# Performance work log

Measured on AMD Instinct MI355X. Metric: run time of the kernel, lower is better.

## Reference

```python
import jax, jax.numpy as jnp
import numpy as np

B, S, N, H, C = 64, 512, 24, 768, 6

CONST_LAST = jnp.array([0.1, 0.1, 0.1, 0.3, 0.8, 0.01], dtype=jnp.float32)
CONST_MID = jnp.array([0.1, 0.1, 0.1, 0.8, 0.3, 0.01], dtype=jnp.float32)


def setup_inputs() -> dict:
    key = jax.random.key(0)
    k1, k2, k3, k4 = jax.random.split(key, 4)
    last_hidden_state = jax.random.normal(k1, (B, S, H), dtype=jnp.float32)
    # strictly increasing boundaries in [0, S-1]: sort randint in [0, S-N) then add arange(N)
    base = jnp.sort(jax.random.randint(k2, (B, N), 0, S - N), axis=1)
    sentence_token = base + jnp.arange(N, dtype=base.dtype)[None, :]
    W = jax.random.normal(k3, (C, H), dtype=jnp.float32) * 0.02
    b = jax.random.normal(k4, (C,), dtype=jnp.float32) * 0.02
    return {"last_hidden_state": last_hidden_state, "sentence_token": sentence_token,
            "W": W, "b": b}


def reference(last_hidden_state, sentence_token, W, b):
    # last_hidden_state: [B,S,H]; sentence_token: [B,N] strictly increasing boundaries.
    # Segment j covers tokens [prev+1, t_j] inclusive (prev = -1 for j==0).
    ends = sentence_token                                            # [B,N]
    prev = jnp.concatenate([-jnp.ones_like(ends[:, :1]), ends[:, :-1]], axis=1)
    # prefix sums with leading zero: csp[:, t+1] = sum of tokens 0..t
    cs = jnp.cumsum(last_hidden_state, axis=1)                       # [B,S,H]
    csp = jnp.concatenate([jnp.zeros_like(cs[:, :1]), cs], axis=1)   # [B,S+1,H]
    seg_sum = (jnp.take_along_axis(csp, (ends + 1)[:, :, None], axis=1)
               - jnp.take_along_axis(csp, (prev + 1)[:, :, None], axis=1))  # [B,N,H]
    lens = (ends - prev).astype(last_hidden_state.dtype)[:, :, None]  # >= 1 by construction
    seg_mean = seg_sum / lens                                         # [B,N,H]
    probs = jax.nn.sigmoid(jnp.einsum('bnh,ch->bnc', seg_mean, W) + b)  # [B,N,C]
    # override: boundary > 500 -> constant probability vector (different if last sentence)
    is_last = (jnp.arange(ends.shape[1]) == ends.shape[1] - 1)[None, :, None]  # [1,N,1]
    const = jnp.where(is_last, CONST_LAST[None, None, :], CONST_MID[None, None, :])
    over = (ends > 500)[:, :, None]
    return jnp.where(over, const, probs)
```

## Files before the change

### kernel.cpp

```cpp
#include <hip/hip_runtime.h>
#include <math.h>

#define B_ 64
#define S_ 512
#define N_ 24
#define H_ 768
#define C_ 6
#define CHUNKS 16
#define TOK_PER_BLOCK (S_ / CHUNKS)
#define TOK_PER_WAVE (TOK_PER_BLOCK / 4)

__global__ __launch_bounds__(256, 4) void seg_proj_kernel(
    const float* __restrict__ lhs, const int* __restrict__ st,
    const float* __restrict__ W, float* __restrict__ outbuf, int use_atomic) {
  __shared__ float acc[N_ * C_ * 64];
  const int tid = threadIdx.x;
  const int lane = tid & 63;
  const int wave = tid >> 6;
  const int b = blockIdx.x / CHUNKS;
  const int chunk = blockIdx.x % CHUNKS;

  float4* accv = (float4*)acc;
#pragma unroll
  for (int i = 0; i < 9; ++i)
    accv[i * 256 + tid] = make_float4(0.f, 0.f, 0.f, 0.f);

  int stb_l = (lane < N_) ? st[b * N_ + lane] : 0x7fffffff;
  const int last = __shfl(stb_l, N_ - 1);
  const int lim = last > 500 ? 500 : last;

  const float4* W4 = (const float4*)W;
  float4 w[3][C_];
#pragma unroll
  for (int k = 0; k < 3; ++k)
#pragma unroll
    for (int c = 0; c < C_; ++c)
      w[k][c] = W4[c * (H_ / 4) + k * 64 + lane];
#pragma unroll
  for (int k = 0; k < 3; ++k)
    asm volatile("" : "+v"(w[k][0].x), "+v"(w[k][0].y), "+v"(w[k][0].z), "+v"(w[k][0].w),
                       "+v"(w[k][1].x), "+v"(w[k][1].y), "+v"(w[k][1].z), "+v"(w[k][1].w),
                       "+v"(w[k][2].x), "+v"(w[k][2].y), "+v"(w[k][2].z), "+v"(w[k][2].w),
                       "+v"(w[k][3].x), "+v"(w[k][3].y), "+v"(w[k][3].z), "+v"(w[k][3].w),
                       "+v"(w[k][4].x), "+v"(w[k][4].y), "+v"(w[k][4].z), "+v"(w[k][4].w),
                       "+v"(w[k][5].x), "+v"(w[k][5].y), "+v"(w[k][5].z), "+v"(w[k][5].w));

  __syncthreads();

  const int s_base = chunk * TOK_PER_BLOCK + wave * TOK_PER_WAVE;
  if (s_base <= lim) {
    const float4* x4 = (const float4*)(lhs + ((size_t)b * S_ + s_base) * H_);
    float4 x[TOK_PER_WAVE][3];
#pragma unroll
    for (int t = 0; t < TOK_PER_WAVE; ++t) {
      x[t][0] = x4[t * 192 + lane];
      x[t][1] = x4[t * 192 + 64 + lane];
      x[t][2] = x4[t * 192 + 128 + lane];
    }

    float racc[C_] = {0.f, 0.f, 0.f, 0.f, 0.f, 0.f};
    int cur_seg = N_;
#pragma unroll
    for (int t = 0; t < TOK_PER_WAVE; ++t) {
      const int s = s_base + t;
      const int seg = (int)__popcll(__ballot(stb_l < s));
      if (seg != cur_seg) {
        if (cur_seg < N_) {
#pragma unroll
        for (int c = 0; c < C_; ++c)
          atomicAdd(&acc[(cur_seg * C_ + c) * 64 + lane], racc[c]);
        }
#pragma unroll
        for (int c = 0; c < C_; ++c) racc[c] = 0.f;
        cur_seg = seg;
      }
#pragma unroll
      for (int k = 0; k < 3; ++k)
#pragma unroll
        for (int c = 0; c < C_; ++c)
          racc[c] += x[t][k].x * w[k][c].x + x[t][k].y * w[k][c].y +
                     x[t][k].z * w[k][c].z + x[t][k].w * w[k][c].w;
    }
    if (cur_seg < N_) {
#pragma unroll
      for (int c = 0; c < C_; ++c)
        atomicAdd(&acc[(cur_seg * C_ + c) * 64 + lane], racc[c]);
    }
  }

  __syncthreads();
  if (tid < N_ * C_) {
    float v = 0.f;
    const int base = tid * 64;
#pragma unroll 8
    for (int i = 0; i < 64; ++i) v += acc[base + ((i + tid) & 63)];
    if (use_atomic)
      atomicAdd(&outbuf[b * N_ * C_ + tid], v);
    else
      outbuf[(size_t)blockIdx.x * (N_ * C_) + tid] = v;
  }
}

__global__ __launch_bounds__(256) void finalize_kernel(
    const float* __restrict__ buf, const int* __restrict__ st,
    const float* __restrict__ bias, float* __restrict__ out, int use_atomic) {
  int idx = blockIdx.x * blockDim.x + threadIdx.x;
  if (idx >= B_ * N_ * C_) return;
  int c = idx % C_;
  int j = (idx / C_) % N_;
  int b = idx / (N_ * C_);
  float ssum;
  if (use_atomic) {
    ssum = buf[idx];
  } else {
    ssum = 0.f;
#pragma unroll
    for (int k = 0; k < CHUNKS; ++k)
      ssum += buf[(size_t)(b * CHUNKS + k) * (N_ * C_) + j * C_ + c];
  }
  int end = st[b * N_ + j];
  int prev = (j == 0) ? -1 : st[b * N_ + j - 1];
  float len = (float)(end - prev);
  float logit = ssum / len + bias[c];
  float p = 1.0f / (1.0f + expf(-logit));
  if (end > 500) {
    float cl = (c < 3) ? 0.1f : (c == 3 ? 0.3f : (c == 4 ? 0.8f : 0.01f));
    float cm = (c < 3) ? 0.1f : (c == 3 ? 0.8f : (c == 4 ? 0.3f : 0.01f));
    p = (j == N_ - 1) ? cl : cm;
  }
  out[idx] = p;
}

extern "C" void kernel_launch(void* const* d_in, const int* in_sizes, int n_in,
                              void* d_out, int out_size, void* d_ws, size_t ws_size,
                              hipStream_t stream) {
  const float* lhs  = (const float*)d_in[0];
  const int*   st   = (const int*)d_in[1];
  const float* W    = (const float*)d_in[2];
  const float* bias = (const float*)d_in[3];

  const size_t need = (size_t)B_ * CHUNKS * N_ * C_ * sizeof(float);
  const int use_atomic = (ws_size < need) ? 1 : 0;
  if (use_atomic)
    hipMemsetAsync(d_ws, 0, (size_t)B_ * N_ * C_ * sizeof(float), stream);

  seg_proj_kernel<<<B_ * CHUNKS, 256, 0, stream>>>(lhs, st, W, (float*)d_ws, use_atomic);
  finalize_kernel<<<(B_ * N_ * C_ + 255) / 256, 256, 0, stream>>>(
      (float*)d_ws, st, bias, (float*)d_out, use_atomic);
}
```

Measured before the change: 184.2 us.

## Fuse finalize into projection kernel via last-block counter and halve chunk count

The separate finalize kernel is merged into the projection kernel: each block writes its partial sums, bumps a per-batch global counter, and the last block for that batch reduces the partials and applies the sigmoid and override. The chunk count drops from 16 to 8, so each wave handles 16 tokens, loaded in two register-bounded halves of 8, with occupancy hint lowered to 2. This removes a kernel launch and the optional memset, at the cost of fewer blocks, more serial work per wave, and dependence on the workspace being large enough with no fallback path.

```diff
diff --git a/kernel.cpp b/kernel.cpp
--- a/kernel.cpp
+++ b/kernel.cpp
@@ -6,19 +6,24 @@
 #define N_ 24
 #define H_ 768
 #define C_ 6
-#define CHUNKS 16
+#define CHUNKS 8
 #define TOK_PER_BLOCK (S_ / CHUNKS)
 #define TOK_PER_WAVE (TOK_PER_BLOCK / 4)
+#define NC (N_ * C_)
 
-__global__ __launch_bounds__(256, 4) void seg_proj_kernel(
+__device__ int g_cnt[B_];
+
+__global__ __launch_bounds__(256, 2) void seg_proj_fused(
     const float* __restrict__ lhs, const int* __restrict__ st,
-    const float* __restrict__ W, float* __restrict__ outbuf, int use_atomic) {
-  __shared__ float acc[N_ * C_ * 64];
+    const float* __restrict__ W, const float* __restrict__ bias,
+    float* __restrict__ ws, float* __restrict__ out) {
+  __shared__ float acc[NC * 64];
+  __shared__ int s_old;
   const int tid = threadIdx.x;
   const int lane = tid & 63;
   const int wave = tid >> 6;
-  const int b = blockIdx.x / CHUNKS;
-  const int chunk = blockIdx.x % CHUNKS;
+  const int b = blockIdx.x >> 3;
+  const int chunk = blockIdx.x & 7;
 
   float4* accv = (float4*)acc;
 #pragma unroll
@@ -48,87 +53,87 @@
   __syncthreads();
 
   const int s_base = chunk * TOK_PER_BLOCK + wave * TOK_PER_WAVE;
-  if (s_base <= lim) {
-    const float4* x4 = (const float4*)(lhs + ((size_t)b * S_ + s_base) * H_);
-    float4 x[TOK_PER_WAVE][3];
+  const float4* x4 = (const float4*)(lhs + ((size_t)b * S_ + s_base) * H_);
+
+  float racc[C_] = {0.f, 0.f, 0.f, 0.f, 0.f, 0.f};
+  int cur_seg = N_;
+#pragma unroll 1
+  for (int h = 0; h < 2; ++h) {
+    const int hb = s_base + h * 8;
+    if (hb <= lim) {
+      float4 x[8][3];
 #pragma unroll
-    for (int t = 0; t < TOK_PER_WAVE; ++t) {
-      x[t][0] = x4[t * 192 + lane];
-      x[t][1] = x4[t * 192 + 64 + lane];
-      x[t][2] = x4[t * 192 + 128 + lane];
-    }
-
-    float racc[C_] = {0.f, 0.f, 0.f, 0.f, 0.f, 0.f};
-    int cur_seg = N_;
+      for (int t = 0; t < 8; ++t) {
+        const int tt = h * 8 + t;
+        x[t][0] = x4[tt * 192 + lane];
+        x[t][1] = x4[tt * 192 + 64 + lane];
+        x[t][2] = x4[tt * 192 + 128 + lane];
+      }
 #pragma unroll
-    for (int t = 0; t < TOK_PER_WAVE; ++t) {
-      const int s = s_base + t;
-      const int seg = (int)__popcll(__ballot(stb_l < s));
-      if (seg != cur_seg) {
-        if (cur_seg < N_) {
+      for (int t = 0; t < 8; ++t) {
+        const int s = hb + t;
+        const int seg = (int)__popcll(__ballot(stb_l < s));
+        if (seg != cur_seg) {
+          if (cur_seg < N_) {
 #pragma unroll
-        for (int c = 0; c < C_; ++c)
-          atomicAdd(&acc[(cur_seg * C_ + c) * 64 + lane], racc[c]);
+            for (int c = 0; c < C_; ++c)
+              atomicAdd(&acc[(cur_seg * C_ + c) * 64 + lane], racc[c]);
+          }
+#pragma unroll
+          for (int c = 0; c < C_; ++c) racc[c] = 0.f;
+          cur_seg = seg;
         }
 #pragma unroll
-        for (int c = 0; c < C_; ++c) racc[c] = 0.f;
-        cur_seg = seg;
+        for (int k = 0; k < 3; ++k)
+#pragma unroll
+          for (int c = 0; c < C_; ++c)
+            racc[c] += x[t][k].x * w[k][c].x + x[t][k].y * w[k][c].y +
+                       x[t][k].z * w[k][c].z + x[t][k].w * w[k][c].w;
       }
+    }
+  }
+  if (cur_seg < N_) {
 #pragma unroll
-      for (int k = 0; k < 3; ++k)
-#pragma unroll
-        for (int c = 0; c < C_; ++c)
-          racc[c] += x[t][k].x * w[k][c].x + x[t][k].y * w[k][c].y +
-                     x[t][k].z * w[k][c].z + x[t][k].w * w[k][c].w;
-    }
-    if (cur_seg < N_) {
-#pragma unroll
-      for (int c = 0; c < C_; ++c)
-        atomicAdd(&acc[(cur_seg * C_ + c) * 64 + lane], racc[c]);
-    }
+    for (int c = 0; c < C_; ++c)
+      atomicAdd(&acc[(cur_seg * C_ + c) * 64 + lane], racc[c]);
   }
 
   __syncthreads();
-  if (tid < N_ * C_) {
+
+  if (tid < NC) {
     float v = 0.f;
     const int base = tid * 64;
 #pragma unroll 8
     for (int i = 0; i < 64; ++i) v += acc[base + ((i + tid) & 63)];
-    if (use_atomic)
-      atomicAdd(&outbuf[b * N_ * C_ + tid], v);
-    else
-      outbuf[(size_t)blockIdx.x * (N_ * C_) + tid] = v;
+    atomicExch(&ws[(size_t)blockIdx.x * NC + tid], v);
   }
-}
 
-__global__ __launch_bounds__(256) void finalize_kernel(
-    const float* __restrict__ buf, const int* __restrict__ st,
-    const float* __restrict__ bias, float* __restrict__ out, int use_atomic) {
-  int idx = blockIdx.x * blockDim.x + threadIdx.x;
-  if (idx >= B_ * N_ * C_) return;
-  int c = idx % C_;
-  int j = (idx / C_) % N_;
-  int b = idx / (N_ * C_);
-  float ssum;
-  if (use_atomic) {
-    ssum = buf[idx];
-  } else {
-    ssum = 0.f;
+  __syncthreads();
+  if (tid == 0) s_old = atomicAdd(&g_cnt[b], 1);
+  __syncthreads();
+
+  if (s_old == CHUNKS - 1) {
+    if (tid < NC) {
+      float* base = ws + (size_t)b * CHUNKS * NC + tid;
+      float ssum = 0.f;
 #pragma unroll
-    for (int k = 0; k < CHUNKS; ++k)
-      ssum += buf[(size_t)(b * CHUNKS + k) * (N_ * C_) + j * C_ + c];
+      for (int k = 0; k < CHUNKS; ++k)
+        ssum += atomicAdd(&base[k * NC], 0.0f);
+      const int c = tid % C_;
+      const int j = tid / C_;
+      const int end = st[b * N_ + j];
+      const int prev = (j == 0) ? -1 : st[b * N_ + j - 1];
+      const float logit = ssum / (float)(end - prev) + bias[c];
+      float p = 1.0f / (1.0f + expf(-logit));
+      if (end > 500) {
+        const float cl = (c < 3) ? 0.1f : (c == 3 ? 0.3f : (c == 4 ? 0.8f : 0.01f));
+        const float cm = (c < 3) ? 0.1f : (c == 3 ? 0.8f : (c == 4 ? 0.3f : 0.01f));
+        p = (j == N_ - 1) ? cl : cm;
+      }
+      out[b * NC + tid] = p;
+    }
+    if (tid == 0) atomicExch(&g_cnt[b], 0);
   }
-  int end = st[b * N_ + j];
-  int prev = (j == 0) ? -1 : st[b * N_ + j - 1];
-  float len = (float)(end - prev);
-  float logit = ssum / len + bias[c];
-  float p = 1.0f / (1.0f + expf(-logit));
-  if (end > 500) {
-    float cl = (c < 3) ? 0.1f : (c == 3 ? 0.3f : (c == 4 ? 0.8f : 0.01f));
-    float cm = (c < 3) ? 0.1f : (c == 3 ? 0.8f : (c == 4 ? 0.3f : 0.01f));
-    p = (j == N_ - 1) ? cl : cm;
-  }
-  out[idx] = p;
 }
 
 extern "C" void kernel_launch(void* const* d_in, const int* in_sizes, int n_in,
@@ -139,12 +144,6 @@
   const float* W    = (const float*)d_in[2];
   const float* bias = (const float*)d_in[3];
 
-  const size_t need = (size_t)B_ * CHUNKS * N_ * C_ * sizeof(float);
-  const int use_atomic = (ws_size < need) ? 1 : 0;
-  if (use_atomic)
-    hipMemsetAsync(d_ws, 0, (size_t)B_ * N_ * C_ * sizeof(float), stream);
-
-  seg_proj_kernel<<<B_ * CHUNKS, 256, 0, stream>>>(lhs, st, W, (float*)d_ws, use_atomic);
-  finalize_kernel<<<(B_ * N_ * C_ + 255) / 256, 256, 0, stream>>>(
-      (float*)d_ws, st, bias, (float*)d_out, use_atomic);
+  seg_proj_fused<<<B_ * CHUNKS, 256, 0, stream>>>(
+      lhs, st, W, bias, (float*)d_ws, (float*)d_out);
 }
```

After: 153.3 us, median of 2. 1.2x faster.
